# Kernel optimization log

Hardware: AMD Instinct MI355X
Metric: run time of the kernel (lower is better)

Reference implementation:

```python
import jax, jax.numpy as jnp
import numpy as np

N = 50000      # nodes
E = 1600000    # edges (avg degree 32)
F_IN = 256     # input feature dim
H = 4          # heads (layers 1,2)
C = 32         # hidden_channels
HC = H * C     # 128
NEG_SLOPE = 0.2


def setup_inputs() -> dict:
    key = jax.random.key(0)
    ks = jax.random.split(key, 18)
    def p(k, shape, scale=0.1):
        return jax.random.normal(k, shape, jnp.float32) * scale
    return {
        "x": jax.random.normal(ks[0], (N, F_IN), jnp.float32),
        "edge_index": jax.random.randint(ks[1], (2, E), 0, N),
        "edge_attr": jax.random.normal(ks[2], (E, 1), jnp.float32),
        # layer 1: 256 -> 4 heads x 32
        "W1": p(ks[3], (F_IN, HC)), "We1": p(ks[4], (1, HC)),
        "as1": p(ks[5], (H, C)), "ad1": p(ks[6], (H, C)), "ae1": p(ks[7], (H, C)),
        "b1": jnp.zeros((HC,), jnp.float32),
        # layer 2: 128 -> 4 heads x 32
        "W2": p(ks[8], (HC, HC)), "We2": p(ks[9], (1, HC)),
        "as2": p(ks[10], (H, C)), "ad2": p(ks[11], (H, C)), "ae2": p(ks[12], (H, C)),
        "b2": jnp.zeros((HC,), jnp.float32),
        # layer 3: 128 -> 1 head x 1
        "W3": p(ks[13], (HC, 1)), "We3": p(ks[14], (1, 1)),
        "as3": p(ks[15], (1, 1)), "ad3": p(ks[16], (1, 1)), "ae3": p(ks[17], (1, 1)),
        "b3": jnp.zeros((1,), jnp.float32),
    }


def _add_self_loops(edge_index, edge_attr, n):
    # PyG GATConv: add_self_loops=True, fill_value='mean' -> self-loop attr is
    # the mean of incoming edge attrs per destination node (0 if none).
    src, dst = edge_index[0], edge_index[1]
    s = jax.ops.segment_sum(edge_attr, dst, num_segments=n)
    cnt = jax.ops.segment_sum(jnp.ones((edge_attr.shape[0], 1), edge_attr.dtype), dst, num_segments=n)
    loop_attr = s / jnp.maximum(cnt, 1.0)
    ar = jnp.arange(n)
    return (jnp.concatenate([src, ar]),
            jnp.concatenate([dst, ar]),
            jnp.concatenate([edge_attr, loop_attr], axis=0))


def _gat(x, src, dst, ea, W, We, a_s, a_d, a_e, b, heads, ch, n):
    h = (x @ W).reshape(-1, heads, ch)    # [n, H, C]
    e = (ea @ We).reshape(-1, heads, ch)  # [Etot, H, C]
    ls = jnp.einsum('nhc,hc->nh', h, a_s)
    ld = jnp.einsum('nhc,hc->nh', h, a_d)
    le = jnp.einsum('ehc,hc->eh', e, a_e)
    logits = jax.nn.leaky_relu(ls[src] + ld[dst] + le, NEG_SLOPE)  # [Etot, H]
    # segment softmax over destination nodes (every node has a self-loop -> no empty segments)
    mx = jax.ops.segment_max(logits, dst, num_segments=n)
    ex = jnp.exp(logits - mx[dst])
    denom = jax.ops.segment_sum(ex, dst, num_segments=n)
    alpha = ex / (denom[dst] + 1e-16)
    out = jax.ops.segment_sum(h[src] * alpha[:, :, None], dst, num_segments=n)  # [n, H, C]
    return out.reshape(n, heads * ch) + b


def reference(x, edge_index, edge_attr,
              W1, We1, as1, ad1, ae1, b1,
              W2, We2, as2, ad2, ae2, b2,
              W3, We3, as3, ad3, ae3, b3):
    n = x.shape[0]
    src, dst, ea = _add_self_loops(edge_index, edge_attr, n)
    h = jax.nn.relu(_gat(x, src, dst, ea, W1, We1, as1, ad1, ae1, b1, H, C, n))
    h = jax.nn.relu(_gat(h, src, dst, ea, W2, We2, as2, ad2, ae2, b2, H, C, n))
    return _gat(h, src, dst, ea, W3, We3, as3, ad3, ae3, b3, 1, 1, n)  # [n, 1]
```

## Files before the change

kernel.cpp:

```cpp
#include <hip/hip_runtime.h>
#include <hip/hip_bf16.h>
#include <hip/hip_fp16.h>

#define NNODES 50000
#define NEDGES 1600000
#define ETOT   (NNODES + NEDGES)
#define FIN    256
#define HC     128
#define NEG    0.2f
#define DEGCAP 128
#define ALP    (DEGCAP + 8)

template <int K>
__device__ __forceinline__ void gemm_body(
        const float* __restrict__ x, const float* __restrict__ W,
        const float* __restrict__ a_s, const float* __restrict__ a_d,
        __half* __restrict__ h, float* __restrict__ ls, float* __restrict__ ld_,
        int n, int bid) {
    constexpr int BM = 64, BK = 32;
    __shared__ float xsT[BK][BM];
    __shared__ float ws[BK][HC];
    int t = threadIdx.x;
    int tx = t & 31;
    int ty = t >> 5;
    int r0 = bid * BM;

    float acc[8][4];
#pragma unroll
    for (int r = 0; r < 8; r++)
#pragma unroll
        for (int c = 0; c < 4; c++) acc[r][c] = 0.f;

    for (int kc = 0; kc < K; kc += BK) {
        __syncthreads();
#pragma unroll
        for (int q = 0; q < 2; q++) {
            int idx = q * 256 + t;
            int m = idx >> 3;
            int k4 = (idx & 7) * 4;
            int row = r0 + m;
            float4 v = (row < n) ? *(const float4*)&x[(size_t)row * K + kc + k4]
                                 : make_float4(0.f, 0.f, 0.f, 0.f);
            float vv[4] = {v.x, v.y, v.z, v.w};
#pragma unroll
            for (int j = 0; j < 4; j++) {
                int k = k4 + j;
                xsT[k][m ^ ((k & 7) << 2)] = vv[j];
            }
        }
#pragma unroll
        for (int q = 0; q < 4; q++) {
            int idx = q * 256 + t;
            int k = idx >> 5;
            int n4 = (idx & 31) * 4;
            *(float4*)&ws[k][n4] = *(const float4*)&W[(size_t)(kc + k) * HC + n4];
        }
        __syncthreads();
#pragma unroll
        for (int kk = 0; kk < BK; kk++) {
            int s = (kk & 7) << 2;
            float4 a0 = *(const float4*)&xsT[kk][(8 * ty) ^ s];
            float4 a1 = *(const float4*)&xsT[kk][(8 * ty + 4) ^ s];
            float4 w0 = *(const float4*)&ws[kk][4 * tx];
            float a[8] = {a0.x, a0.y, a0.z, a0.w, a1.x, a1.y, a1.z, a1.w};
            float wv[4] = {w0.x, w0.y, w0.z, w0.w};
#pragma unroll
            for (int r = 0; r < 8; r++)
#pragma unroll
                for (int c = 0; c < 4; c++)
                    acc[r][c] = fmaf(a[r], wv[c], acc[r][c]);
        }
    }

    int head = tx >> 3;
    float4 sa4 = *(const float4*)&a_s[4 * tx];
    float4 sd4 = *(const float4*)&a_d[4 * tx];
    float sa[4] = {sa4.x, sa4.y, sa4.z, sa4.w};
    float sd[4] = {sd4.x, sd4.y, sd4.z, sd4.w};
#pragma unroll
    for (int r = 0; r < 8; r++) {
        int row = r0 + 8 * ty + r;
        if (row >= n) break;
        union { __half2 h2[2]; int2 i2; } u;
        u.h2[0] = __floats2half2_rn(acc[r][0], acc[r][1]);
        u.h2[1] = __floats2half2_rn(acc[r][2], acc[r][3]);
        *(int2*)&h[(size_t)row * HC + 4 * tx] = u.i2;
        float p = acc[r][0] * sa[0] + acc[r][1] * sa[1] + acc[r][2] * sa[2] + acc[r][3] * sa[3];
        float q = acc[r][0] * sd[0] + acc[r][1] * sd[1] + acc[r][2] * sd[2] + acc[r][3] * sd[3];
        p += __shfl_xor(p, 1); q += __shfl_xor(q, 1);
        p += __shfl_xor(p, 2); q += __shfl_xor(q, 2);
        p += __shfl_xor(p, 4); q += __shfl_xor(q, 4);
        if ((tx & 7) == 0) {
            ls[row * 4 + head] = p;
            ld_[row * 4 + head] = q;
        }
    }
}

__global__ __launch_bounds__(256) void gemm1_rank_fused(
        const float* __restrict__ x, const float* __restrict__ W,
        const float* __restrict__ a_s, const float* __restrict__ a_d,
        __half* __restrict__ h, float* __restrict__ ls, float* __restrict__ ld_,
        int n,
        const int* __restrict__ ei, int* __restrict__ rank, int* __restrict__ deg, int E,
        const float* We1, const float* ae1, const float* We2, const float* ae2,
        const float* We3, const float* ae3, float* __restrict__ wedot,
        int gB, int rB) {
    int b = blockIdx.x;
    if (b < gB) {
        gemm_body<FIN>(x, W, a_s, a_d, h, ls, ld_, n, b);
    } else if (b < gB + rB) {
        int i = (b - gB) * 256 + threadIdx.x;
        if (i < E) rank[i] = atomicAdd(&deg[ei[E + i]], 1);
    } else {
        int t = threadIdx.x;
        if (t < 128) {
            float p1 = We1[t] * ae1[t];
            float p2 = We2[t] * ae2[t];
            for (int o = 16; o; o >>= 1) {
                p1 += __shfl_xor(p1, o, 32);
                p2 += __shfl_xor(p2, o, 32);
            }
            if ((t & 31) == 0) {
                wedot[t >> 5] = p1;
                wedot[4 + (t >> 5)] = p2;
            }
            if (t == 0) wedot[8] = We3[0] * ae3[0];
        }
    }
}

template <int K>
__global__ __launch_bounds__(256) void gemm_lsld(
        const float* __restrict__ x, const float* __restrict__ W,
        const float* __restrict__ a_s, const float* __restrict__ a_d,
        __half* __restrict__ h, float* __restrict__ ls, float* __restrict__ ld_,
        int n) {
    gemm_body<K>(x, W, a_s, a_d, h, ls, ld_, n, blockIdx.x);
}


__global__ void scan_block(const int* __restrict__ deg, int* __restrict__ out,
                           int* __restrict__ bsum, int n) {
    __shared__ int sh[256];
    int t = threadIdx.x;
    int i = blockIdx.x * 256 + t;
    int v = (i < n) ? (deg[i] + 1) : 0;
    sh[t] = v;
    __syncthreads();
    for (int o = 1; o < 256; o <<= 1) {
        int a = (t >= o) ? sh[t - o] : 0;
        __syncthreads();
        sh[t] += a;
        __syncthreads();
    }
    if (i < n) out[i] = sh[t] - v;
    if (t == 255) bsum[blockIdx.x] = sh[255];
}

__global__ void scan_top(int* __restrict__ bsum, int nb) {
    __shared__ int sh[256];
    int t = threadIdx.x;
    int v = (t < nb) ? bsum[t] : 0;
    sh[t] = v;
    __syncthreads();
    for (int o = 1; o < 256; o <<= 1) {
        int a = (t >= o) ? sh[t - o] : 0;
        __syncthreads();
        sh[t] += a;
        __syncthreads();
    }
    if (t < nb) bsum[t] = sh[t] - v;
}

__global__ void scan_add(int* __restrict__ rp, const int* __restrict__ boff,
                         int n, int etot) {
    int i = blockIdx.x * blockDim.x + threadIdx.x;
    if (i < n)      rp[i] += boff[i >> 8];
    else if (i == n) rp[n] = etot;
}

__global__ void scatter_k(const int* __restrict__ ei, const float* __restrict__ ea,
                          const int* __restrict__ rp, const int* __restrict__ rank,
                          int2* __restrict__ csr, int E) {
    int i = blockIdx.x * blockDim.x + threadIdx.x;
    if (i < E) {
        int d = ei[E + i];
        int pos = rp[d] + rank[i];
        csr[pos] = make_int2(ei[i], __float_as_int(ea[i]));
    }
}

__global__ __launch_bounds__(256) void selfloop_k(const int* __restrict__ rp,
                                                  int2* __restrict__ csr, int n) {
    int idx = blockIdx.x * blockDim.x + threadIdx.x;
    int node = idx >> 3, l = idx & 7;
    if (node >= n) return;
    int beg = rp[node], end = rp[node + 1] - 1;
    float s = 0.f;
    for (int j = beg + l; j < end; j += 8) s += __int_as_float(csr[j].y);
    s += __shfl_xor(s, 1, 8);
    s += __shfl_xor(s, 2, 8);
    s += __shfl_xor(s, 4, 8);
    if (l == 0)
        csr[end] = make_int2(node, __float_as_int(s / fmaxf((float)(end - beg), 1.0f)));
}

template <bool RELU, bool FUSE3>
__global__ __launch_bounds__(128) void agg_k(
        const __half* __restrict__ h, const float* __restrict__ ls,
        const float* __restrict__ ld_, const int* __restrict__ row_ptr,
        const int2* __restrict__ csr,
        const float* __restrict__ wedot, const float* __restrict__ bias,
        float* __restrict__ out, const float* __restrict__ W3,
        float* __restrict__ h3, int n) {
    __shared__ float albuf[4][ALP];
    __shared__ int srcbuf[DEGCAP];
    __shared__ float pacc[8][HC];
    __shared__ float hsuminv[4];
    int nid = blockIdx.x;
    int t = threadIdx.x, head = t >> 5, lane = t & 31;
    int beg = row_ptr[nid], end = row_ptr[nid + 1];
    int deg = end - beg;
    float ldn = ld_[nid * 4 + head];
    float wd = wedot[head];

    float v;
    if (deg <= DEGCAP) {
        float lgr[4];
        float mx = -1e30f;
#pragma unroll
        for (int i = 0; i < 4; i++) {
            int e = lane + 32 * i;
            float lg = -1e30f;
            if (e < deg) {
                int2 ce = csr[beg + e];
                if (head == 0) srcbuf[e] = ce.x << 8;
                lg = ls[ce.x * 4 + head] + ldn + __int_as_float(ce.y) * wd;
                lg = lg > 0.f ? lg : NEG * lg;
            }
            lgr[i] = lg;
            mx = fmaxf(mx, lg);
        }
        for (int o = 16; o; o >>= 1) mx = fmaxf(mx, __shfl_xor(mx, o, 32));

        float sum = 0.f;
#pragma unroll
        for (int i = 0; i < 4; i++) {
            int e = lane + 32 * i;
            if (e < deg) {
                float p = __expf(lgr[i] - mx);
                albuf[head][e] = p;
                sum += p;
            }
        }
        for (int o = 16; o; o >>= 1) sum += __shfl_xor(sum, o, 32);
        if (lane == 0) hsuminv[head] = 1.f / (sum + 1e-16f);
        __syncthreads();

        int g = t >> 4, l = t & 15;
        int c0 = 8 * l;
        const float* al = albuf[c0 >> 5];
        const char* hb = (const char*)h + 16 * l;
        float acc[8];
#pragma unroll
        for (int j = 0; j < 8; j++) acc[j] = 0.f;
        int e = g;
        for (; e + 8 < deg; e += 16) {
            int o0 = srcbuf[e], o1 = srcbuf[e + 8];
            int4 r0 = *(const int4*)(hb + o0);
            int4 r1 = *(const int4*)(hb + o1);
            float a0 = al[e], a1 = al[e + 8];
            const __half2* p0 = (const __half2*)&r0;
            const __half2* p1 = (const __half2*)&r1;
#pragma unroll
            for (int j = 0; j < 4; j++) {
                float2 f0 = __half22float2(p0[j]);
                float2 f1 = __half22float2(p1[j]);
                acc[2 * j]     = fmaf(a0, f0.x, acc[2 * j]);
                acc[2 * j + 1] = fmaf(a0, f0.y, acc[2 * j + 1]);
                acc[2 * j]     = fmaf(a1, f1.x, acc[2 * j]);
                acc[2 * j + 1] = fmaf(a1, f1.y, acc[2 * j + 1]);
            }
        }
        for (; e < deg; e += 8) {
            int o0 = srcbuf[e];
            int4 r0 = *(const int4*)(hb + o0);
            float a0 = al[e];
            const __half2* p0 = (const __half2*)&r0;
#pragma unroll
            for (int j = 0; j < 4; j++) {
                float2 f0 = __half22float2(p0[j]);
                acc[2 * j]     = fmaf(a0, f0.x, acc[2 * j]);
                acc[2 * j + 1] = fmaf(a0, f0.y, acc[2 * j + 1]);
            }
        }
#pragma unroll
        for (int j = 0; j < 4; j++)
            *(float2*)&pacc[g][c0 + 2 * j] = make_float2(acc[2 * j], acc[2 * j + 1]);
        __syncthreads();

        float inv = hsuminv[head];
        float sv = pacc[0][t];
#pragma unroll
        for (int g2 = 1; g2 < 8; g2++) sv += pacc[g2][t];
        v = sv * inv + bias[t];
    } else {
        float mx = -1e30f;
        for (int j = beg + lane; j < end; j += 32) {
            int2 ce = csr[j];
            float lg = ls[ce.x * 4 + head] + ldn + __int_as_float(ce.y) * wd;
            lg = lg > 0.f ? lg : NEG * lg;
            mx = fmaxf(mx, lg);
        }
        for (int o = 16; o; o >>= 1) mx = fmaxf(mx, __shfl_xor(mx, o, 32));
        float sum = 0.f, acc = 0.f;
        for (int j = beg; j < end; j++) {
            int2 ce = csr[j];
            float lg = ls[ce.x * 4 + head] + ldn + __int_as_float(ce.y) * wd;
            lg = lg > 0.f ? lg : NEG * lg;
            float p = __expf(lg - mx);
            sum += p;
            acc = fmaf(p, __half2float(h[(size_t)ce.x * HC + t]), acc);
        }
        v = acc / (sum + 1e-16f) + bias[t];
    }

    if (RELU) v = fmaxf(v, 0.f);
    if (!FUSE3) out[(size_t)nid * HC + t] = v;

    if (FUSE3) {
        float p = v * W3[t];
        for (int o = 32; o; o >>= 1) p += __shfl_xor(p, o, 64);
        __shared__ float sh[2];
        if ((t & 63) == 0) sh[t >> 6] = p;
        __syncthreads();
        if (t == 0) h3[nid] = sh[0] + sh[1];
    }
}

__global__ __launch_bounds__(256) void layer3_k(
        const float* __restrict__ h3, const int* __restrict__ row_ptr,
        const int2* __restrict__ csr,
        const float* __restrict__ wedot, const float* __restrict__ as3,
        const float* __restrict__ ad3, const float* __restrict__ b3,
        float* __restrict__ out, int n) {
    int idx = blockIdx.x * blockDim.x + threadIdx.x;
    int node = idx >> 3, l = idx & 7;
    if (node >= n) return;
    float A = as3[0], D = ad3[0], wd = wedot[8];
    int beg = row_ptr[node], end = row_ptr[node + 1];
    float hdn = h3[node] * D;

    float mx = -1e30f;
    for (int j = beg + l; j < end; j += 8) {
        int2 ce = csr[j];
        float lg = h3[ce.x] * A + hdn + __int_as_float(ce.y) * wd;
        lg = lg > 0.f ? lg : NEG * lg;
        mx = fmaxf(mx, lg);
    }
    mx = fmaxf(mx, __shfl_xor(mx, 1, 8));
    mx = fmaxf(mx, __shfl_xor(mx, 2, 8));
    mx = fmaxf(mx, __shfl_xor(mx, 4, 8));

    float sum = 0.f, num = 0.f;
    for (int j = beg + l; j < end; j += 8) {
        int2 ce = csr[j];
        float hv = h3[ce.x];
        float lg = hv * A + hdn + __int_as_float(ce.y) * wd;
        lg = lg > 0.f ? lg : NEG * lg;
        float p = __expf(lg - mx);
        sum += p;
        num = fmaf(p, hv, num);
    }
    sum += __shfl_xor(sum, 1, 8); num += __shfl_xor(num, 1, 8);
    sum += __shfl_xor(sum, 2, 8); num += __shfl_xor(num, 2, 8);
    sum += __shfl_xor(sum, 4, 8); num += __shfl_xor(num, 4, 8);
    if (l == 0) out[node] = num / (sum + 1e-16f) + b3[0];
}


extern "C" void kernel_launch(void* const* d_in, const int* in_sizes, int n_in,
                              void* d_out, int out_size, void* d_ws, size_t ws_size,
                              hipStream_t stream) {
    const float* x   = (const float*)d_in[0];
    const int*   ei  = (const int*)d_in[1];
    const float* ea  = (const float*)d_in[2];
    const float* W1  = (const float*)d_in[3];
    const float* We1 = (const float*)d_in[4];
    const float* as1 = (const float*)d_in[5];
    const float* ad1 = (const float*)d_in[6];
    const float* ae1 = (const float*)d_in[7];
    const float* b1  = (const float*)d_in[8];
    const float* W2  = (const float*)d_in[9];
    const float* We2 = (const float*)d_in[10];
    const float* as2 = (const float*)d_in[11];
    const float* ad2 = (const float*)d_in[12];
    const float* ae2 = (const float*)d_in[13];
    const float* b2  = (const float*)d_in[14];
    const float* W3  = (const float*)d_in[15];
    const float* We3 = (const float*)d_in[16];
    const float* as3 = (const float*)d_in[17];
    const float* ad3 = (const float*)d_in[18];
    const float* ae3 = (const float*)d_in[19];
    const float* b3  = (const float*)d_in[20];

    const int N = NNODES, E = NEDGES, etot = ETOT;

    char* ws = (char*)d_ws;
    size_t o = 0;
    auto alloc = [&](size_t bytes) { size_t r = o; o = (o + bytes + 255) & ~(size_t)255; return r; };
    size_t o_deg   = alloc((size_t)N * 4);
    size_t zero_span = o;
    size_t o_rp    = alloc((size_t)(N + 1) * 4);
    size_t o_bsum  = alloc(256 * 4);
    size_t o_wd    = alloc(16 * 4);
    size_t o_rank  = alloc((size_t)E * 4);
    size_t o_csr   = alloc((size_t)etot * 8);
    size_t o_ls    = alloc((size_t)N * 4 * 4);
    size_t o_ld    = alloc((size_t)N * 4 * 4);
    size_t o_h3    = alloc((size_t)N * 4);
    size_t o_h16   = alloc((size_t)N * HC * 2);
    size_t o_bufB  = alloc((size_t)N * HC * 4);

    int*    deg   = (int*)(ws + o_deg);
    int*    rp    = (int*)(ws + o_rp);
    int*    bsum  = (int*)(ws + o_bsum);
    float*  wd    = (float*)(ws + o_wd);
    int*    rank  = (int*)(ws + o_rank);
    int2*   csr   = (int2*)(ws + o_csr);
    float*  ls    = (float*)(ws + o_ls);
    float*  ld_   = (float*)(ws + o_ld);
    float*  h3    = (float*)(ws + o_h3);
    __half* h16   = (__half*)(ws + o_h16);
    float*  bufB  = (float*)(ws + o_bufB);

    hipMemsetAsync(ws, 0, zero_span, stream);

    int gB = (N + 63) / 64;
    int rB = (E + 255) / 256;
    int nb = (N + 255) / 256;

    gemm1_rank_fused<<<gB + rB + 1, 256, 0, stream>>>(
        x, W1, as1, ad1, h16, ls, ld_, N,
        ei, rank, deg, E,
        We1, ae1, We2, ae2, We3, ae3, wd, gB, rB);

    scan_block<<<nb, 256, 0, stream>>>(deg, rp, bsum, N);
    scan_top<<<1, 256, 0, stream>>>(bsum, nb);
    scan_add<<<(N + 256) / 256, 256, 0, stream>>>(rp, bsum, N, etot);
    scatter_k<<<(E + 255) / 256, 256, 0, stream>>>(ei, ea, rp, rank, csr, E);
    selfloop_k<<<(N * 8 + 255) / 256, 256, 0, stream>>>(rp, csr, N);

    agg_k<true, false><<<N, 128, 0, stream>>>(h16, ls, ld_, rp, csr, wd, b1,
                                              bufB, nullptr, nullptr, N);
    gemm_lsld<HC><<<(N + 63) / 64, 256, 0, stream>>>(bufB, W2, as2, ad2, h16, ls, ld_, N);
    agg_k<true, true><<<N, 128, 0, stream>>>(h16, ls, ld_, rp, csr, wd + 4, b2,
                                             nullptr, W3, h3, N);
    layer3_k<<<(N * 8 + 255) / 256, 256, 0, stream>>>(h3, rp, csr, wd, as3, ad3, b3,
                                                      (float*)d_out, N);
}
```

Measured before the change: 303.3 us.

## Fuse self-loop attr into aggregation, store layer-1 output fp16, shrink rank array

Removes the separate self-loop kernel by computing the mean edge attribute for each node inside the aggregation and layer-3 kernels. The first aggregation writes fp16 features, which the second GEMM reads directly. The edge rank array becomes 16-bit. The aggregation softmax is reorganised to one thread per edge covering all four heads, with block-level reductions. This cuts kernel launches and memory traffic, at the cost of reduced precision in the intermediate activations and a rank that overflows past 65535 in-degree.

```diff
diff --git a/kernel.cpp b/kernel.cpp
--- a/kernel.cpp
+++ b/kernel.cpp
@@ -11,9 +11,9 @@
 #define DEGCAP 128
 #define ALP    (DEGCAP + 8)
 
-template <int K>
+template <int K, bool XH>
 __device__ __forceinline__ void gemm_body(
-        const float* __restrict__ x, const float* __restrict__ W,
+        const void* __restrict__ xv, const float* __restrict__ W,
         const float* __restrict__ a_s, const float* __restrict__ a_d,
         __half* __restrict__ h, float* __restrict__ ls, float* __restrict__ ld_,
         int n, int bid) {
@@ -39,9 +39,19 @@
             int m = idx >> 3;
             int k4 = (idx & 7) * 4;
             int row = r0 + m;
-            float4 v = (row < n) ? *(const float4*)&x[(size_t)row * K + kc + k4]
-                                 : make_float4(0.f, 0.f, 0.f, 0.f);
-            float vv[4] = {v.x, v.y, v.z, v.w};
+            float vv[4] = {0.f, 0.f, 0.f, 0.f};
+            if (row < n) {
+                if constexpr (XH) {
+                    const __half* xh = (const __half*)xv;
+                    int2 rw = *(const int2*)&xh[(size_t)row * K + kc + k4];
+                    float2 f0 = __half22float2(*reinterpret_cast<const __half2*>(&rw.x));
+                    float2 f1 = __half22float2(*reinterpret_cast<const __half2*>(&rw.y));
+                    vv[0] = f0.x; vv[1] = f0.y; vv[2] = f1.x; vv[3] = f1.y;
+                } else {
+                    float4 vt = *(const float4*)&((const float*)xv)[(size_t)row * K + kc + k4];
+                    vv[0] = vt.x; vv[1] = vt.y; vv[2] = vt.z; vv[3] = vt.w;
+                }
+            }
 #pragma unroll
             for (int j = 0; j < 4; j++) {
                 int k = k4 + j;
@@ -102,16 +112,17 @@
         const float* __restrict__ a_s, const float* __restrict__ a_d,
         __half* __restrict__ h, float* __restrict__ ls, float* __restrict__ ld_,
         int n,
-        const int* __restrict__ ei, int* __restrict__ rank, int* __restrict__ deg, int E,
+        const int* __restrict__ ei, unsigned short* __restrict__ rank,
+        int* __restrict__ deg, int E,
         const float* We1, const float* ae1, const float* We2, const float* ae2,
         const float* We3, const float* ae3, float* __restrict__ wedot,
         int gB, int rB) {
     int b = blockIdx.x;
     if (b < gB) {
-        gemm_body<FIN>(x, W, a_s, a_d, h, ls, ld_, n, b);
+        gemm_body<FIN, false>(x, W, a_s, a_d, h, ls, ld_, n, b);
     } else if (b < gB + rB) {
         int i = (b - gB) * 256 + threadIdx.x;
-        if (i < E) rank[i] = atomicAdd(&deg[ei[E + i]], 1);
+        if (i < E) rank[i] = (unsigned short)atomicAdd(&deg[ei[E + i]], 1);
     } else {
         int t = threadIdx.x;
         if (t < 128) {
@@ -130,13 +141,13 @@
     }
 }
 
-template <int K>
+template <int K, bool XH>
 __global__ __launch_bounds__(256) void gemm_lsld(
-        const float* __restrict__ x, const float* __restrict__ W,
+        const void* __restrict__ x, const float* __restrict__ W,
         const float* __restrict__ a_s, const float* __restrict__ a_d,
         __half* __restrict__ h, float* __restrict__ ls, float* __restrict__ ld_,
         int n) {
-    gemm_body<K>(x, W, a_s, a_d, h, ls, ld_, n, blockIdx.x);
+    gemm_body<K, XH>(x, W, a_s, a_d, h, ls, ld_, n, blockIdx.x);
 }
 
 
@@ -181,29 +192,14 @@
 }
 
 __global__ void scatter_k(const int* __restrict__ ei, const float* __restrict__ ea,
-                          const int* __restrict__ rp, const int* __restrict__ rank,
+                          const int* __restrict__ rp, const unsigned short* __restrict__ rank,
                           int2* __restrict__ csr, int E) {
     int i = blockIdx.x * blockDim.x + threadIdx.x;
     if (i < E) {
         int d = ei[E + i];
-        int pos = rp[d] + rank[i];
+        int pos = rp[d] + (int)rank[i];
         csr[pos] = make_int2(ei[i], __float_as_int(ea[i]));
     }
-}
-
-__global__ __launch_bounds__(256) void selfloop_k(const int* __restrict__ rp,
-                                                  int2* __restrict__ csr, int n) {
-    int idx = blockIdx.x * blockDim.x + threadIdx.x;
-    int node = idx >> 3, l = idx & 7;
-    if (node >= n) return;
-    int beg = rp[node], end = rp[node + 1] - 1;
-    float s = 0.f;
-    for (int j = beg + l; j < end; j += 8) s += __int_as_float(csr[j].y);
-    s += __shfl_xor(s, 1, 8);
-    s += __shfl_xor(s, 2, 8);
-    s += __shfl_xor(s, 4, 8);
-    if (l == 0)
-        csr[end] = make_int2(node, __float_as_int(s / fmaxf((float)(end - beg), 1.0f)));
 }
 
 template <bool RELU, bool FUSE3>
@@ -212,51 +208,90 @@
         const float* __restrict__ ld_, const int* __restrict__ row_ptr,
         const int2* __restrict__ csr,
         const float* __restrict__ wedot, const float* __restrict__ bias,
-        float* __restrict__ out, const float* __restrict__ W3,
+        __half* __restrict__ out, const float* __restrict__ W3,
         float* __restrict__ h3, int n) {
     __shared__ float albuf[4][ALP];
     __shared__ int srcbuf[DEGCAP];
     __shared__ float pacc[8][HC];
-    __shared__ float hsuminv[4];
+    __shared__ float redA[2];
+    __shared__ float redM[2][4];
+    __shared__ float redS[2][4];
     int nid = blockIdx.x;
-    int t = threadIdx.x, head = t >> 5, lane = t & 31;
+    int t = threadIdx.x;
     int beg = row_ptr[nid], end = row_ptr[nid + 1];
     int deg = end - beg;
-    float ldn = ld_[nid * 4 + head];
-    float wd = wedot[head];
 
     float v;
     if (deg <= DEGCAP) {
-        float lgr[4];
-        float mx = -1e30f;
-#pragma unroll
-        for (int i = 0; i < 4; i++) {
-            int e = lane + 32 * i;
-            float lg = -1e30f;
-            if (e < deg) {
-                int2 ce = csr[beg + e];
-                if (head == 0) srcbuf[e] = ce.x << 8;
-                lg = ls[ce.x * 4 + head] + ldn + __int_as_float(ce.y) * wd;
-                lg = lg > 0.f ? lg : NEG * lg;
-            }
-            lgr[i] = lg;
-            mx = fmaxf(mx, lg);
-        }
-        for (int o = 16; o; o >>= 1) mx = fmaxf(mx, __shfl_xor(mx, o, 32));
-
-        float sum = 0.f;
-#pragma unroll
-        for (int i = 0; i < 4; i++) {
-            int e = lane + 32 * i;
-            if (e < deg) {
-                float p = __expf(lgr[i] - mx);
-                albuf[head][e] = p;
-                sum += p;
-            }
-        }
-        for (int o = 16; o; o >>= 1) sum += __shfl_xor(sum, o, 32);
-        if (lane == 0) hsuminv[head] = 1.f / (sum + 1e-16f);
-        __syncthreads();
+        int degr = deg - 1;
+        int src = nid;
+        float eav = 0.f;
+        if (t < degr) {
+            int2 ce = csr[beg + t];
+            src = ce.x;
+            eav = __int_as_float(ce.y);
+        }
+        float es = (t < degr) ? eav : 0.f;
+#pragma unroll
+        for (int o = 32; o; o >>= 1) es += __shfl_xor(es, o, 64);
+        if ((t & 63) == 0) redA[t >> 6] = es;
+        __syncthreads();
+        es = redA[0] + redA[1];
+        if (t == degr) eav = es / fmaxf((float)degr, 1.f);
+
+        float4 wd4 = *(const float4*)wedot;
+        float4 ldn4 = *(const float4*)&ld_[nid * 4];
+        float lg0, lg1, lg2, lg3;
+        if (t < deg) {
+            float4 ls4 = *(const float4*)&ls[src * 4];
+            lg0 = ls4.x + ldn4.x + eav * wd4.x; lg0 = lg0 > 0.f ? lg0 : NEG * lg0;
+            lg1 = ls4.y + ldn4.y + eav * wd4.y; lg1 = lg1 > 0.f ? lg1 : NEG * lg1;
+            lg2 = ls4.z + ldn4.z + eav * wd4.z; lg2 = lg2 > 0.f ? lg2 : NEG * lg2;
+            lg3 = ls4.w + ldn4.w + eav * wd4.w; lg3 = lg3 > 0.f ? lg3 : NEG * lg3;
+            srcbuf[t] = src << 8;
+        } else {
+            lg0 = lg1 = lg2 = lg3 = -1e30f;
+        }
+        float m0 = lg0, m1 = lg1, m2 = lg2, m3 = lg3;
+#pragma unroll
+        for (int o = 32; o; o >>= 1) {
+            m0 = fmaxf(m0, __shfl_xor(m0, o, 64));
+            m1 = fmaxf(m1, __shfl_xor(m1, o, 64));
+            m2 = fmaxf(m2, __shfl_xor(m2, o, 64));
+            m3 = fmaxf(m3, __shfl_xor(m3, o, 64));
+        }
+        if ((t & 63) == 0) {
+            redM[t >> 6][0] = m0; redM[t >> 6][1] = m1;
+            redM[t >> 6][2] = m2; redM[t >> 6][3] = m3;
+        }
+        __syncthreads();
+        m0 = fmaxf(redM[0][0], redM[1][0]);
+        m1 = fmaxf(redM[0][1], redM[1][1]);
+        m2 = fmaxf(redM[0][2], redM[1][2]);
+        m3 = fmaxf(redM[0][3], redM[1][3]);
+        float s0 = 0.f, s1 = 0.f, s2 = 0.f, s3 = 0.f;
+        if (t < deg) {
+            s0 = __expf(lg0 - m0); albuf[0][t] = s0;
+            s1 = __expf(lg1 - m1); albuf[1][t] = s1;
+            s2 = __expf(lg2 - m2); albuf[2][t] = s2;
+            s3 = __expf(lg3 - m3); albuf[3][t] = s3;
+        }
+#pragma unroll
+        for (int o = 32; o; o >>= 1) {
+            s0 += __shfl_xor(s0, o, 64);
+            s1 += __shfl_xor(s1, o, 64);
+            s2 += __shfl_xor(s2, o, 64);
+            s3 += __shfl_xor(s3, o, 64);
+        }
+        if ((t & 63) == 0) {
+            redS[t >> 6][0] = s0; redS[t >> 6][1] = s1;
+            redS[t >> 6][2] = s2; redS[t >> 6][3] = s3;
+        }
+        __syncthreads();
+        s0 = redS[0][0] + redS[1][0];
+        s1 = redS[0][1] + redS[1][1];
+        s2 = redS[0][2] + redS[1][2];
+        s3 = redS[0][3] + redS[1][3];
 
         int g = t >> 4, l = t & 15;
         int c0 = 8 * l;
@@ -300,22 +335,38 @@
             *(float2*)&pacc[g][c0 + 2 * j] = make_float2(acc[2 * j], acc[2 * j + 1]);
         __syncthreads();
 
-        float inv = hsuminv[head];
+        int head = t >> 5;
+        float sumh = (head == 0) ? s0 : (head == 1) ? s1 : (head == 2) ? s2 : s3;
+        float inv = 1.f / (sumh + 1e-16f);
         float sv = pacc[0][t];
 #pragma unroll
         for (int g2 = 1; g2 < 8; g2++) sv += pacc[g2][t];
         v = sv * inv + bias[t];
     } else {
-        float mx = -1e30f;
-        for (int j = beg + lane; j < end; j += 32) {
+        int head = t >> 5, lane = t & 31;
+        float ldn = ld_[nid * 4 + head];
+        float wd = wedot[head];
+        int endr = end - 1;
+        float easum = 0.f, mx = -1e30f;
+        for (int j = beg + lane; j < endr; j += 32) {
             int2 ce = csr[j];
-            float lg = ls[ce.x * 4 + head] + ldn + __int_as_float(ce.y) * wd;
+            float eav = __int_as_float(ce.y);
+            easum += eav;
+            float lg = ls[ce.x * 4 + head] + ldn + eav * wd;
             lg = lg > 0.f ? lg : NEG * lg;
             mx = fmaxf(mx, lg);
         }
-        for (int o = 16; o; o >>= 1) mx = fmaxf(mx, __shfl_xor(mx, o, 32));
-        float sum = 0.f, acc = 0.f;
-        for (int j = beg; j < end; j++) {
+        for (int o = 16; o; o >>= 1) {
+            easum += __shfl_xor(easum, o, 32);
+            mx = fmaxf(mx, __shfl_xor(mx, o, 32));
+        }
+        float mean = easum / fmaxf((float)(endr - beg), 1.f);
+        float lgs = ls[nid * 4 + head] + ldn + mean * wd;
+        lgs = lgs > 0.f ? lgs : NEG * lgs;
+        mx = fmaxf(mx, lgs);
+        float sum = __expf(lgs - mx);
+        float acc = sum * __half2float(h[(size_t)nid * HC + t]);
+        for (int j = beg; j < endr; j++) {
             int2 ce = csr[j];
             float lg = ls[ce.x * 4 + head] + ldn + __int_as_float(ce.y) * wd;
             lg = lg > 0.f ? lg : NEG * lg;
@@ -327,7 +378,7 @@
     }
 
     if (RELU) v = fmaxf(v, 0.f);
-    if (!FUSE3) out[(size_t)nid * HC + t] = v;
+    if (!FUSE3) out[(size_t)nid * HC + t] = __float2half(v);
 
     if (FUSE3) {
         float p = v * W3[t];
@@ -349,22 +400,29 @@
     int node = idx >> 3, l = idx & 7;
     if (node >= n) return;
     float A = as3[0], D = ad3[0], wd = wedot[8];
-    int beg = row_ptr[node], end = row_ptr[node + 1];
-    float hdn = h3[node] * D;
-
-    float mx = -1e30f;
-    for (int j = beg + l; j < end; j += 8) {
+    int beg = row_ptr[node], endr = row_ptr[node + 1] - 1;
+    float hs = h3[node];
+    float hdn = hs * D;
+
+    float easum = 0.f, mx = -1e30f;
+    for (int j = beg + l; j < endr; j += 8) {
         int2 ce = csr[j];
-        float lg = h3[ce.x] * A + hdn + __int_as_float(ce.y) * wd;
+        float eav = __int_as_float(ce.y);
+        easum += eav;
+        float lg = h3[ce.x] * A + hdn + eav * wd;
         lg = lg > 0.f ? lg : NEG * lg;
         mx = fmaxf(mx, lg);
     }
-    mx = fmaxf(mx, __shfl_xor(mx, 1, 8));
-    mx = fmaxf(mx, __shfl_xor(mx, 2, 8));
-    mx = fmaxf(mx, __shfl_xor(mx, 4, 8));
+    easum += __shfl_xor(easum, 1, 8); mx = fmaxf(mx, __shfl_xor(mx, 1, 8));
+    easum += __shfl_xor(easum, 2, 8); mx = fmaxf(mx, __shfl_xor(mx, 2, 8));
+    easum += __shfl_xor(easum, 4, 8); mx = fmaxf(mx, __shfl_xor(mx, 4, 8));
+    float mean = easum / fmaxf((float)(endr - beg), 1.f);
+    float lgs = hs * A + hdn + mean * wd;
+    lgs = lgs > 0.f ? lgs : NEG * lgs;
+    mx = fmaxf(mx, lgs);
 
     float sum = 0.f, num = 0.f;
-    for (int j = beg + l; j < end; j += 8) {
+    for (int j = beg + l; j < endr; j += 8) {
         int2 ce = csr[j];
         float hv = h3[ce.x];
         float lg = hv * A + hdn + __int_as_float(ce.y) * wd;
@@ -376,7 +434,12 @@
     sum += __shfl_xor(sum, 1, 8); num += __shfl_xor(num, 1, 8);
     sum += __shfl_xor(sum, 2, 8); num += __shfl_xor(num, 2, 8);
     sum += __shfl_xor(sum, 4, 8); num += __shfl_xor(num, 4, 8);
-    if (l == 0) out[node] = num / (sum + 1e-16f) + b3[0];
+    if (l == 0) {
+        float p = __expf(lgs - mx);
+        sum += p;
+        num = fmaf(p, hs, num);
+        out[node] = num / (sum + 1e-16f) + b3[0];
+    }
 }
 
 
@@ -415,25 +478,25 @@
     size_t o_rp    = alloc((size_t)(N + 1) * 4);
     size_t o_bsum  = alloc(256 * 4);
     size_t o_wd    = alloc(16 * 4);
-    size_t o_rank  = alloc((size_t)E * 4);
+    size_t o_rank  = alloc((size_t)E * 2);
     size_t o_csr   = alloc((size_t)etot * 8);
     size_t o_ls    = alloc((size_t)N * 4 * 4);
     size_t o_ld    = alloc((size_t)N * 4 * 4);
     size_t o_h3    = alloc((size_t)N * 4);
     size_t o_h16   = alloc((size_t)N * HC * 2);
-    size_t o_bufB  = alloc((size_t)N * HC * 4);
-
-    int*    deg   = (int*)(ws + o_deg);
-    int*    rp    = (int*)(ws + o_rp);
-    int*    bsum  = (int*)(ws + o_bsum);
-    float*  wd    = (float*)(ws + o_wd);
-    int*    rank  = (int*)(ws + o_rank);
-    int2*   csr   = (int2*)(ws + o_csr);
-    float*  ls    = (float*)(ws + o_ls);
-    float*  ld_   = (float*)(ws + o_ld);
-    float*  h3    = (float*)(ws + o_h3);
-    __half* h16   = (__half*)(ws + o_h16);
-    float*  bufB  = (float*)(ws + o_bufB);
+    size_t o_h16b  = alloc((size_t)N * HC * 2);
+
+    int*            deg   = (int*)(ws + o_deg);
+    int*            rp    = (int*)(ws + o_rp);
+    int*            bsum  = (int*)(ws + o_bsum);
+    float*          wd    = (float*)(ws + o_wd);
+    unsigned short* rank  = (unsigned short*)(ws + o_rank);
+    int2*           csr   = (int2*)(ws + o_csr);
+    float*          ls    = (float*)(ws + o_ls);
+    float*          ld_   = (float*)(ws + o_ld);
+    float*          h3    = (float*)(ws + o_h3);
+    __half*         h16   = (__half*)(ws + o_h16);
+    __half*         h16b  = (__half*)(ws + o_h16b);
 
     hipMemsetAsync(ws, 0, zero_span, stream);
 
@@ -450,11 +513,11 @@
     scan_top<<<1, 256, 0, stream>>>(bsum, nb);
     scan_add<<<(N + 256) / 256, 256, 0, stream>>>(rp, bsum, N, etot);
     scatter_k<<<(E + 255) / 256, 256, 0, stream>>>(ei, ea, rp, rank, csr, E);
-    selfloop_k<<<(N * 8 + 255) / 256, 256, 0, stream>>>(rp, csr, N);
 
     agg_k<true, false><<<N, 128, 0, stream>>>(h16, ls, ld_, rp, csr, wd, b1,
-                                              bufB, nullptr, nullptr, N);
-    gemm_lsld<HC><<<(N + 63) / 64, 256, 0, stream>>>(bufB, W2, as2, ad2, h16, ls, ld_, N);
+                                              h16b, nullptr, nullptr, N);
+    gemm_lsld<HC, true><<<(N + 63) / 64, 256, 0, stream>>>(h16b, W2, as2, ad2,
+                                                           h16, ls, ld_, N);
     agg_k<true, true><<<N, 128, 0, stream>>>(h16, ls, ld_, rp, csr, wd + 4, b2,
                                              nullptr, W3, h3, N);
     layer3_k<<<(N * 8 + 255) / 256, 256, 0, stream>>>(h3, rp, csr, wd, as3, ad3, b3,
```

After: 330.8 us. +9.1%, slower.
